# Performance work log

Measured on AMD Instinct MI355X. Metric: run time of the kernel, lower is better.

The kernel has to match this reference:

```python
import jax, jax.numpy as jnp
import numpy as np

B, T, C, HS = 4, 2048, 1024, 64  # batch, seq, n_embd, head_size


def setup_inputs() -> dict:
    key = jax.random.key(0)
    k1, k2, k3, k4 = jax.random.split(key, 4)
    x = jax.random.normal(k1, (B, T, C), dtype=jnp.float32)
    Wq = jax.random.normal(k2, (HS, C), dtype=jnp.float32) * (C ** -0.5)
    Wk = jax.random.normal(k3, (HS, C), dtype=jnp.float32) * (C ** -0.5)
    Wv = jax.random.normal(k4, (HS, C), dtype=jnp.float32) * (C ** -0.5)
    return {"x": x, "Wq": Wq, "Wk": Wk, "Wv": Wv}


def reference(x, Wq, Wk, Wv):
    # q,k,v: [B,T,HS] (nn.Linear: x @ W.T, no bias)
    q = jnp.einsum('btc,hc->bth', x, Wq)
    k = jnp.einsum('btc,hc->bth', x, Wk)
    v = jnp.einsum('btc,hc->bth', x, Wv)
    scale = k.shape[-1] ** -0.5
    wei = jnp.einsum('bth,bsh->bts', q, k) * scale  # [B,T,T]
    # causal mask (tril == 0 -> -inf)
    mask = jnp.tril(jnp.ones((T, T), dtype=bool))
    wei = jnp.where(mask, wei, -jnp.inf)
    wei = jax.nn.softmax(wei, axis=-1)
    # dropout p=0.0 -> identity
    out = jnp.einsum('bts,bsh->bth', wei, v)  # [B,T,HS]
    return out
```

## Files before the change

kernel.cpp:

```cpp
#include <hip/hip_runtime.h>
#include <hip/hip_bf16.h>

#define BB 4
#define TT 2048
#define CC 1024
#define HSZ 64
#define NTOT 8192

typedef __attribute__((ext_vector_type(8))) short bf16x8;
typedef __attribute__((ext_vector_type(4))) float f32x4;

__device__ __forceinline__ unsigned short f2bf(float x) {
    __hip_bfloat16 h = __float2bfloat16(x);
    return *reinterpret_cast<unsigned short*>(&h);
}
__device__ __forceinline__ float bf2f(unsigned short u) {
    return __uint_as_float(((unsigned int)u) << 16);
}

__global__ __launch_bounds__(256) void convert_w(
    const float* __restrict__ Wq, const float* __restrict__ Wk,
    const float* __restrict__ Wv, unsigned short* __restrict__ Wh) {
    int i = blockIdx.x * 256 + threadIdx.x;
    if (i >= 192 * 1024) return;
    int c = i >> 10, kk = i & 1023;
    float val;
    if (c < 64) val = Wq[(size_t)c * CC + kk] * 0.125f;
    else if (c < 128) val = Wk[(size_t)(c - 64) * CC + kk];
    else val = Wv[(size_t)(c - 128) * CC + kk];
    Wh[i] = f2bf(val);
}

__global__ __launch_bounds__(256, 2) void qkv_mfma(
    const float* __restrict__ x, const unsigned short* __restrict__ Wh,
    unsigned short* __restrict__ qs, unsigned short* __restrict__ ksb,
    unsigned short* __restrict__ vT) {
    __shared__ __align__(16) float Pt[4 * 16 * 196];

    const int tid = threadIdx.x;
    const int w = tid >> 6, lane = tid & 63;
    const int l16 = lane & 15, quad = lane >> 4;
    const int row0 = blockIdx.x * 16;
    const int Arow = row0 + l16;

    f32x4 acc[12];
#pragma unroll
    for (int t = 0; t < 12; ++t) acc[t] = (f32x4){0.f, 0.f, 0.f, 0.f};

#pragma unroll
    for (int ch = 0; ch < 4; ++ch) {
        const int kb = w * 256 + ch * 64;
        const float* xp = x + (size_t)Arow * CC + kb;
        float4 xa = *(const float4*)&xp[quad * 8];
        float4 xb = *(const float4*)&xp[quad * 8 + 4];
        float4 xc = *(const float4*)&xp[32 + quad * 8];
        float4 xd = *(const float4*)&xp[32 + quad * 8 + 4];
        bf16x8 ah0, al0, ah1, al1;
        {
            float v0[8] = {xa.x, xa.y, xa.z, xa.w, xb.x, xb.y, xb.z, xb.w};
            float v1[8] = {xc.x, xc.y, xc.z, xc.w, xd.x, xd.y, xd.z, xd.w};
#pragma unroll
            for (int j = 0; j < 8; ++j) {
                unsigned short h = f2bf(v0[j]);
                ah0[j] = (short)h;
                al0[j] = (short)f2bf(v0[j] - bf2f(h));
                unsigned short h2 = f2bf(v1[j]);
                ah1[j] = (short)h2;
                al1[j] = (short)f2bf(v1[j] - bf2f(h2));
            }
        }
#pragma unroll
        for (int nt = 0; nt < 12; ++nt) {
            const unsigned short* Wp = &Wh[(size_t)(nt * 16 + l16) * CC + kb + quad * 8];
            bf16x8 b0 = *(const bf16x8*)Wp;
            bf16x8 b1 = *(const bf16x8*)(Wp + 32);
            f32x4 a = acc[nt];
            a = __builtin_amdgcn_mfma_f32_16x16x32_bf16(ah0, b0, a, 0, 0, 0);
            a = __builtin_amdgcn_mfma_f32_16x16x32_bf16(al0, b0, a, 0, 0, 0);
            a = __builtin_amdgcn_mfma_f32_16x16x32_bf16(ah1, b1, a, 0, 0, 0);
            a = __builtin_amdgcn_mfma_f32_16x16x32_bf16(al1, b1, a, 0, 0, 0);
            acc[nt] = a;
        }
    }
#pragma unroll
    for (int nt = 0; nt < 12; ++nt)
#pragma unroll
        for (int r = 0; r < 4; ++r)
            Pt[(w * 16 + quad * 4 + r) * 196 + nt * 16 + l16] = acc[nt][r];
    __syncthreads();
    for (int e = tid; e < 16 * 192; e += 256) {
        const int row = e / 192, col = e - row * 192;
        float s = 0.f;
#pragma unroll
        for (int kk = 0; kk < 4; ++kk) s += Pt[(kk * 16 + row) * 196 + col];
        unsigned short h = f2bf(s);
        const int grow = row0 + row;
        if (col < 64) qs[(size_t)grow * HSZ + col] = h;
        else if (col < 128) ksb[(size_t)grow * HSZ + (col - 64)] = h;
        else vT[(size_t)(col - 128) * NTOT + grow] = h;
    }
}

__global__ __launch_bounds__(256, 2) void attn_mfma(
    const unsigned short* __restrict__ qs, const unsigned short* __restrict__ ksb,
    const unsigned short* __restrict__ vT, float* __restrict__ out) {
    __shared__ __align__(16) unsigned char smem[17664];
    unsigned short* Ps = (unsigned short*)smem;
    float* Om = (float*)smem;
    float* Lm = (float*)(smem + 17408);

    const int raw = blockIdx.x;
    const int i = (raw < 256) ? raw : 767 - raw;
    const int b = i >> 7;
    const int qt = i & 127;
    const int t0 = qt * 16;
    const int tid = threadIdx.x;
    const int w = tid >> 6, lane = tid & 63;
    const int l16 = lane & 15, quad = lane >> 4;

    const size_t qoff = (size_t)(b * TT + t0 + l16) * HSZ + quad * 8;
    const bf16x8 aq0 = *(const bf16x8*)&qs[qoff];
    const bf16x8 aq1 = *(const bf16x8*)&qs[qoff + 32];

    f32x4 OC[4];
#pragma unroll
    for (int t = 0; t < 4; ++t) OC[t] = (f32x4){0.f, 0.f, 0.f, 0.f};
    float lsum[4] = {0.f, 0.f, 0.f, 0.f};

    const unsigned short* kbase = ksb + (size_t)b * TT * HSZ;
    const int nk = (qt >> 2) + 1;

    bf16x8 ck0[4], ck1[4];
    if (w < nk) {
        const int key0 = w * 64;
#pragma unroll
        for (int nt = 0; nt < 4; ++nt) {
            const unsigned short* kp = kbase + (size_t)(key0 + nt * 16 + l16) * HSZ + quad * 8;
            ck0[nt] = *(const bf16x8*)kp;
            ck1[nt] = *(const bf16x8*)(kp + 32);
        }
    }

    for (int j = w; j < nk; j += 4) {
        const int key0 = j * 64;
        bf16x8 cv0[4], cv1[4];
#pragma unroll
        for (int ht = 0; ht < 4; ++ht) {
            const unsigned short* vp = vT + (size_t)(ht * 16 + l16) * NTOT + b * TT + key0 + quad * 8;
            cv0[ht] = *(const bf16x8*)vp;
            cv1[ht] = *(const bf16x8*)(vp + 32);
        }
        bf16x8 nk0[4], nk1[4];
        const bool more = (j + 4) < nk;
        if (more) {
            const int key0n = key0 + 256;
#pragma unroll
            for (int nt = 0; nt < 4; ++nt) {
                const unsigned short* kp = kbase + (size_t)(key0n + nt * 16 + l16) * HSZ + quad * 8;
                nk0[nt] = *(const bf16x8*)kp;
                nk1[nt] = *(const bf16x8*)(kp + 32);
            }
        }
        f32x4 S[4];
#pragma unroll
        for (int nt = 0; nt < 4; ++nt) {
            f32x4 a = (f32x4){0.f, 0.f, 0.f, 0.f};
            a = __builtin_amdgcn_mfma_f32_16x16x32_bf16(aq0, ck0[nt], a, 0, 0, 0);
            a = __builtin_amdgcn_mfma_f32_16x16x32_bf16(aq1, ck1[nt], a, 0, 0, 0);
            S[nt] = a;
        }
        if (j == nk - 1) {
#pragma unroll
            for (int nt = 0; nt < 4; ++nt) {
                const int key = key0 + nt * 16 + l16;
#pragma unroll
                for (int r = 0; r < 4; ++r)
                    if (key > t0 + quad * 4 + r) S[nt][r] = -1e30f;
            }
        }
#pragma unroll
        for (int nt = 0; nt < 4; ++nt)
#pragma unroll
            for (int r = 0; r < 4; ++r) S[nt][r] = __expf(S[nt][r]);
#pragma unroll
        for (int r = 0; r < 4; ++r)
            lsum[r] += S[0][r] + S[1][r] + S[2][r] + S[3][r];
        unsigned short* Pw = Ps + w * 1152;
#pragma unroll
        for (int nt = 0; nt < 4; ++nt)
#pragma unroll
            for (int r = 0; r < 4; ++r)
                Pw[(quad * 4 + r) * 72 + nt * 16 + l16] = f2bf(S[nt][r]);
        bf16x8 pf0 = *(const bf16x8*)&Pw[l16 * 72 + quad * 8];
        bf16x8 pf1 = *(const bf16x8*)&Pw[l16 * 72 + 32 + quad * 8];
#pragma unroll
        for (int ht = 0; ht < 4; ++ht) {
            f32x4 a = OC[ht];
            a = __builtin_amdgcn_mfma_f32_16x16x32_bf16(pf0, cv0[ht], a, 0, 0, 0);
            a = __builtin_amdgcn_mfma_f32_16x16x32_bf16(pf1, cv1[ht], a, 0, 0, 0);
            OC[ht] = a;
        }
        if (more) {
#pragma unroll
            for (int nt = 0; nt < 4; ++nt) { ck0[nt] = nk0[nt]; ck1[nt] = nk1[nt]; }
        }
    }
#pragma unroll
    for (int r = 0; r < 4; ++r) {
        float v = lsum[r];
#pragma unroll
        for (int off = 1; off < 16; off <<= 1) v += __shfl_xor(v, off, 64);
        lsum[r] = v;
    }
    __syncthreads();
#pragma unroll
    for (int ht = 0; ht < 4; ++ht)
#pragma unroll
        for (int r = 0; r < 4; ++r)
            Om[(w * 16 + quad * 4 + r) * 68 + ht * 16 + l16] = OC[ht][r];
    if (l16 == 0) {
#pragma unroll
        for (int r = 0; r < 4; ++r) Lm[w * 16 + quad * 4 + r] = lsum[r];
    }
    __syncthreads();
    {
        const int row = tid >> 4, h0 = (tid & 15) * 4;
        float L = 0.f, o0 = 0.f, o1 = 0.f, o2 = 0.f, o3 = 0.f;
#pragma unroll
        for (int w2 = 0; w2 < 4; ++w2) {
            L += Lm[w2 * 16 + row];
            const float* p = &Om[(w2 * 16 + row) * 68 + h0];
            o0 += p[0]; o1 += p[1]; o2 += p[2]; o3 += p[3];
        }
        const float inv = 1.f / L;
        *(float4*)&out[(size_t)(b * TT + t0 + row) * HSZ + h0] =
            (float4){o0 * inv, o1 * inv, o2 * inv, o3 * inv};
    }
}

extern "C" void kernel_launch(void* const* d_in, const int* in_sizes, int n_in,
                              void* d_out, int out_size, void* d_ws, size_t ws_size,
                              hipStream_t stream) {
    const float* x  = (const float*)d_in[0];
    const float* Wq = (const float*)d_in[1];
    const float* Wk = (const float*)d_in[2];
    const float* Wv = (const float*)d_in[3];
    float* out = (float*)d_out;

    unsigned short* qs = (unsigned short*)d_ws;
    unsigned short* ksb = qs + (size_t)NTOT * HSZ;
    unsigned short* vT = ksb + (size_t)NTOT * HSZ;
    unsigned short* Wh = vT + (size_t)NTOT * HSZ;

    convert_w<<<768, 256, 0, stream>>>(Wq, Wk, Wv, Wh);
    qkv_mfma<<<512, 256, 0, stream>>>(x, Wh, qs, ksb, vT);
    attn_mfma<<<512, 256, 0, stream>>>(qs, ksb, vT, out);
}
```

Measured before the change: 120.4 us.

## Fuse weight conversion, QKV projection and attention into one cooperative kernel

Merges the three kernels into a single cooperative launch, with grid-wide syncs between weight conversion, QKV projection and attention, to remove two kernel launch gaps. The attention stage also drops the register double-buffered prefetch of K tiles and loads K inline, which lowers register pressure. The costs are grid.sync overhead, a larger shared allocation (50 KB) sized for the projection stage, and a cooperative launch that requires all 512 blocks to be resident at once.

```diff
diff --git a/kernel.cpp b/kernel.cpp
--- a/kernel.cpp
+++ b/kernel.cpp
@@ -1,5 +1,8 @@
 #include <hip/hip_runtime.h>
 #include <hip/hip_bf16.h>
+#include <hip/hip_cooperative_groups.h>
+
+namespace cg = cooperative_groups;
 
 #define BB 4
 #define TT 2048
@@ -18,223 +21,203 @@
     return __uint_as_float(((unsigned int)u) << 16);
 }
 
-__global__ __launch_bounds__(256) void convert_w(
-    const float* __restrict__ Wq, const float* __restrict__ Wk,
-    const float* __restrict__ Wv, unsigned short* __restrict__ Wh) {
-    int i = blockIdx.x * 256 + threadIdx.x;
-    if (i >= 192 * 1024) return;
-    int c = i >> 10, kk = i & 1023;
-    float val;
-    if (c < 64) val = Wq[(size_t)c * CC + kk] * 0.125f;
-    else if (c < 128) val = Wk[(size_t)(c - 64) * CC + kk];
-    else val = Wv[(size_t)(c - 128) * CC + kk];
-    Wh[i] = f2bf(val);
-}
-
-__global__ __launch_bounds__(256, 2) void qkv_mfma(
-    const float* __restrict__ x, const unsigned short* __restrict__ Wh,
+__global__ __launch_bounds__(256, 2) void fused_head(
+    const float* __restrict__ x, const float* __restrict__ Wq,
+    const float* __restrict__ Wk, const float* __restrict__ Wv,
     unsigned short* __restrict__ qs, unsigned short* __restrict__ ksb,
-    unsigned short* __restrict__ vT) {
-    __shared__ __align__(16) float Pt[4 * 16 * 196];
+    unsigned short* __restrict__ vT, unsigned short* __restrict__ Wh,
+    float* __restrict__ out) {
+    __shared__ __align__(16) unsigned char smem[50176];
+    cg::grid_group grid = cg::this_grid();
 
     const int tid = threadIdx.x;
     const int w = tid >> 6, lane = tid & 63;
     const int l16 = lane & 15, quad = lane >> 4;
-    const int row0 = blockIdx.x * 16;
-    const int Arow = row0 + l16;
-
-    f32x4 acc[12];
-#pragma unroll
-    for (int t = 0; t < 12; ++t) acc[t] = (f32x4){0.f, 0.f, 0.f, 0.f};
-
-#pragma unroll
-    for (int ch = 0; ch < 4; ++ch) {
-        const int kb = w * 256 + ch * 64;
-        const float* xp = x + (size_t)Arow * CC + kb;
-        float4 xa = *(const float4*)&xp[quad * 8];
-        float4 xb = *(const float4*)&xp[quad * 8 + 4];
-        float4 xc = *(const float4*)&xp[32 + quad * 8];
-        float4 xd = *(const float4*)&xp[32 + quad * 8 + 4];
-        bf16x8 ah0, al0, ah1, al1;
+
+    for (int i = blockIdx.x * 256 + tid; i < 192 * 1024; i += 512 * 256) {
+        const int c = i >> 10, kk = i & 1023;
+        float val;
+        if (c < 64) val = Wq[(size_t)c * CC + kk] * 0.125f;
+        else if (c < 128) val = Wk[(size_t)(c - 64) * CC + kk];
+        else val = Wv[(size_t)(c - 128) * CC + kk];
+        Wh[i] = f2bf(val);
+    }
+    __threadfence();
+    grid.sync();
+
+    {
+        float* Pt = (float*)smem;
+        const int row0 = blockIdx.x * 16;
+        const int Arow = row0 + l16;
+
+        f32x4 acc[12];
+#pragma unroll
+        for (int t = 0; t < 12; ++t) acc[t] = (f32x4){0.f, 0.f, 0.f, 0.f};
+
+#pragma unroll
+        for (int ch = 0; ch < 4; ++ch) {
+            const int kb = w * 256 + ch * 64;
+            const float* xp = x + (size_t)Arow * CC + kb;
+            float4 xa = *(const float4*)&xp[quad * 8];
+            float4 xb = *(const float4*)&xp[quad * 8 + 4];
+            float4 xc = *(const float4*)&xp[32 + quad * 8];
+            float4 xd = *(const float4*)&xp[32 + quad * 8 + 4];
+            bf16x8 ah0, al0, ah1, al1;
+            {
+                float v0[8] = {xa.x, xa.y, xa.z, xa.w, xb.x, xb.y, xb.z, xb.w};
+                float v1[8] = {xc.x, xc.y, xc.z, xc.w, xd.x, xd.y, xd.z, xd.w};
+#pragma unroll
+                for (int j = 0; j < 8; ++j) {
+                    unsigned short h = f2bf(v0[j]);
+                    ah0[j] = (short)h;
+                    al0[j] = (short)f2bf(v0[j] - bf2f(h));
+                    unsigned short h2 = f2bf(v1[j]);
+                    ah1[j] = (short)h2;
+                    al1[j] = (short)f2bf(v1[j] - bf2f(h2));
+                }
+            }
+#pragma unroll
+            for (int nt = 0; nt < 12; ++nt) {
+                const unsigned short* Wp = &Wh[(size_t)(nt * 16 + l16) * CC + kb + quad * 8];
+                bf16x8 b0 = *(const bf16x8*)Wp;
+                bf16x8 b1 = *(const bf16x8*)(Wp + 32);
+                f32x4 a = acc[nt];
+                a = __builtin_amdgcn_mfma_f32_16x16x32_bf16(ah0, b0, a, 0, 0, 0);
+                a = __builtin_amdgcn_mfma_f32_16x16x32_bf16(al0, b0, a, 0, 0, 0);
+                a = __builtin_amdgcn_mfma_f32_16x16x32_bf16(ah1, b1, a, 0, 0, 0);
+                a = __builtin_amdgcn_mfma_f32_16x16x32_bf16(al1, b1, a, 0, 0, 0);
+                acc[nt] = a;
+            }
+        }
+#pragma unroll
+        for (int nt = 0; nt < 12; ++nt)
+#pragma unroll
+            for (int r = 0; r < 4; ++r)
+                Pt[(w * 16 + quad * 4 + r) * 196 + nt * 16 + l16] = acc[nt][r];
+        __syncthreads();
+        for (int e = tid; e < 16 * 192; e += 256) {
+            const int row = e / 192, col = e - row * 192;
+            float s = 0.f;
+#pragma unroll
+            for (int kk = 0; kk < 4; ++kk) s += Pt[(kk * 16 + row) * 196 + col];
+            unsigned short h = f2bf(s);
+            const int grow = row0 + row;
+            if (col < 64) qs[(size_t)grow * HSZ + col] = h;
+            else if (col < 128) ksb[(size_t)grow * HSZ + (col - 64)] = h;
+            else vT[(size_t)(col - 128) * NTOT + grow] = h;
+        }
+    }
+    __threadfence();
+    grid.sync();
+
+    {
+        unsigned short* Ps = (unsigned short*)smem;
+        float* Om = (float*)smem;
+        float* Lm = (float*)(smem + 17408);
+
+        const int raw = blockIdx.x;
+        const int i = (raw < 256) ? raw : 767 - raw;
+        const int b = i >> 7;
+        const int qt = i & 127;
+        const int t0 = qt * 16;
+
+        const size_t qoff = (size_t)(b * TT + t0 + l16) * HSZ + quad * 8;
+        const bf16x8 aq0 = *(const bf16x8*)&qs[qoff];
+        const bf16x8 aq1 = *(const bf16x8*)&qs[qoff + 32];
+
+        f32x4 OC[4];
+#pragma unroll
+        for (int t = 0; t < 4; ++t) OC[t] = (f32x4){0.f, 0.f, 0.f, 0.f};
+        float lsum[4] = {0.f, 0.f, 0.f, 0.f};
+
+        const unsigned short* kbase = ksb + (size_t)b * TT * HSZ;
+        const int nk = (qt >> 2) + 1;
+
+        for (int j = w; j < nk; j += 4) {
+            const int key0 = j * 64;
+            bf16x8 cv0[4], cv1[4];
+#pragma unroll
+            for (int ht = 0; ht < 4; ++ht) {
+                const unsigned short* vp =
+                    vT + (size_t)(ht * 16 + l16) * NTOT + b * TT + key0 + quad * 8;
+                cv0[ht] = *(const bf16x8*)vp;
+                cv1[ht] = *(const bf16x8*)(vp + 32);
+            }
+            f32x4 S[4];
+#pragma unroll
+            for (int nt = 0; nt < 4; ++nt) {
+                const unsigned short* kp =
+                    kbase + (size_t)(key0 + nt * 16 + l16) * HSZ + quad * 8;
+                bf16x8 bk0 = *(const bf16x8*)kp;
+                bf16x8 bk1 = *(const bf16x8*)(kp + 32);
+                f32x4 a = (f32x4){0.f, 0.f, 0.f, 0.f};
+                a = __builtin_amdgcn_mfma_f32_16x16x32_bf16(aq0, bk0, a, 0, 0, 0);
+                a = __builtin_amdgcn_mfma_f32_16x16x32_bf16(aq1, bk1, a, 0, 0, 0);
+                S[nt] = a;
+            }
+            if (j == nk - 1) {
+#pragma unroll
+                for (int nt = 0; nt < 4; ++nt) {
+                    const int key = key0 + nt * 16 + l16;
+#pragma unroll
+                    for (int r = 0; r < 4; ++r)
+                        if (key > t0 + quad * 4 + r) S[nt][r] = -1e30f;
+                }
+            }
+#pragma unroll
+            for (int nt = 0; nt < 4; ++nt)
+#pragma unroll
+                for (int r = 0; r < 4; ++r) S[nt][r] = __expf(S[nt][r]);
+#pragma unroll
+            for (int r = 0; r < 4; ++r)
+                lsum[r] += S[0][r] + S[1][r] + S[2][r] + S[3][r];
+            unsigned short* Pw = Ps + w * 1152;
+#pragma unroll
+            for (int nt = 0; nt < 4; ++nt)
+#pragma unroll
+                for (int r = 0; r < 4; ++r)
+                    Pw[(quad * 4 + r) * 72 + nt * 16 + l16] = f2bf(S[nt][r]);
+            bf16x8 pf0 = *(const bf16x8*)&Pw[l16 * 72 + quad * 8];
+            bf16x8 pf1 = *(const bf16x8*)&Pw[l16 * 72 + 32 + quad * 8];
+#pragma unroll
+            for (int ht = 0; ht < 4; ++ht) {
+                f32x4 a = OC[ht];
+                a = __builtin_amdgcn_mfma_f32_16x16x32_bf16(pf0, cv0[ht], a, 0, 0, 0);
+                a = __builtin_amdgcn_mfma_f32_16x16x32_bf16(pf1, cv1[ht], a, 0, 0, 0);
+                OC[ht] = a;
+            }
+        }
+#pragma unroll
+        for (int r = 0; r < 4; ++r) {
+            float v = lsum[r];
+#pragma unroll
+            for (int off = 1; off < 16; off <<= 1) v += __shfl_xor(v, off, 64);
+            lsum[r] = v;
+        }
+        __syncthreads();
+#pragma unroll
+        for (int ht = 0; ht < 4; ++ht)
+#pragma unroll
+            for (int r = 0; r < 4; ++r)
+                Om[(w * 16 + quad * 4 + r) * 68 + ht * 16 + l16] = OC[ht][r];
+        if (l16 == 0) {
+#pragma unroll
+            for (int r = 0; r < 4; ++r) Lm[w * 16 + quad * 4 + r] = lsum[r];
+        }
+        __syncthreads();
         {
-            float v0[8] = {xa.x, xa.y, xa.z, xa.w, xb.x, xb.y, xb.z, xb.w};
-            float v1[8] = {xc.x, xc.y, xc.z, xc.w, xd.x, xd.y, xd.z, xd.w};
-#pragma unroll
-            for (int j = 0; j < 8; ++j) {
-                unsigned short h = f2bf(v0[j]);
-                ah0[j] = (short)h;
-                al0[j] = (short)f2bf(v0[j] - bf2f(h));
-                unsigned short h2 = f2bf(v1[j]);
-                ah1[j] = (short)h2;
-                al1[j] = (short)f2bf(v1[j] - bf2f(h2));
-            }
-        }
-#pragma unroll
-        for (int nt = 0; nt < 12; ++nt) {
-            const unsigned short* Wp = &Wh[(size_t)(nt * 16 + l16) * CC + kb + quad * 8];
-            bf16x8 b0 = *(const bf16x8*)Wp;
-            bf16x8 b1 = *(const bf16x8*)(Wp + 32);
-            f32x4 a = acc[nt];
-            a = __builtin_amdgcn_mfma_f32_16x16x32_bf16(ah0, b0, a, 0, 0, 0);
-            a = __builtin_amdgcn_mfma_f32_16x16x32_bf16(al0, b0, a, 0, 0, 0);
-            a = __builtin_amdgcn_mfma_f32_16x16x32_bf16(ah1, b1, a, 0, 0, 0);
-            a = __builtin_amdgcn_mfma_f32_16x16x32_bf16(al1, b1, a, 0, 0, 0);
-            acc[nt] = a;
-        }
-    }
-#pragma unroll
-    for (int nt = 0; nt < 12; ++nt)
-#pragma unroll
-        for (int r = 0; r < 4; ++r)
-            Pt[(w * 16 + quad * 4 + r) * 196 + nt * 16 + l16] = acc[nt][r];
-    __syncthreads();
-    for (int e = tid; e < 16 * 192; e += 256) {
-        const int row = e / 192, col = e - row * 192;
-        float s = 0.f;
-#pragma unroll
-        for (int kk = 0; kk < 4; ++kk) s += Pt[(kk * 16 + row) * 196 + col];
-        unsigned short h = f2bf(s);
-        const int grow = row0 + row;
-        if (col < 64) qs[(size_t)grow * HSZ + col] = h;
-        else if (col < 128) ksb[(size_t)grow * HSZ + (col - 64)] = h;
-        else vT[(size_t)(col - 128) * NTOT + grow] = h;
-    }
-}
-
-__global__ __launch_bounds__(256, 2) void attn_mfma(
-    const unsigned short* __restrict__ qs, const unsigned short* __restrict__ ksb,
-    const unsigned short* __restrict__ vT, float* __restrict__ out) {
-    __shared__ __align__(16) unsigned char smem[17664];
-    unsigned short* Ps = (unsigned short*)smem;
-    float* Om = (float*)smem;
-    float* Lm = (float*)(smem + 17408);
-
-    const int raw = blockIdx.x;
-    const int i = (raw < 256) ? raw : 767 - raw;
-    const int b = i >> 7;
-    const int qt = i & 127;
-    const int t0 = qt * 16;
-    const int tid = threadIdx.x;
-    const int w = tid >> 6, lane = tid & 63;
-    const int l16 = lane & 15, quad = lane >> 4;
-
-    const size_t qoff = (size_t)(b * TT + t0 + l16) * HSZ + quad * 8;
-    const bf16x8 aq0 = *(const bf16x8*)&qs[qoff];
-    const bf16x8 aq1 = *(const bf16x8*)&qs[qoff + 32];
-
-    f32x4 OC[4];
-#pragma unroll
-    for (int t = 0; t < 4; ++t) OC[t] = (f32x4){0.f, 0.f, 0.f, 0.f};
-    float lsum[4] = {0.f, 0.f, 0.f, 0.f};
-
-    const unsigned short* kbase = ksb + (size_t)b * TT * HSZ;
-    const int nk = (qt >> 2) + 1;
-
-    bf16x8 ck0[4], ck1[4];
-    if (w < nk) {
-        const int key0 = w * 64;
-#pragma unroll
-        for (int nt = 0; nt < 4; ++nt) {
-            const unsigned short* kp = kbase + (size_t)(key0 + nt * 16 + l16) * HSZ + quad * 8;
-            ck0[nt] = *(const bf16x8*)kp;
-            ck1[nt] = *(const bf16x8*)(kp + 32);
-        }
-    }
-
-    for (int j = w; j < nk; j += 4) {
-        const int key0 = j * 64;
-        bf16x8 cv0[4], cv1[4];
-#pragma unroll
-        for (int ht = 0; ht < 4; ++ht) {
-            const unsigned short* vp = vT + (size_t)(ht * 16 + l16) * NTOT + b * TT + key0 + quad * 8;
-            cv0[ht] = *(const bf16x8*)vp;
-            cv1[ht] = *(const bf16x8*)(vp + 32);
-        }
-        bf16x8 nk0[4], nk1[4];
-        const bool more = (j + 4) < nk;
-        if (more) {
-            const int key0n = key0 + 256;
-#pragma unroll
-            for (int nt = 0; nt < 4; ++nt) {
-                const unsigned short* kp = kbase + (size_t)(key0n + nt * 16 + l16) * HSZ + quad * 8;
-                nk0[nt] = *(const bf16x8*)kp;
-                nk1[nt] = *(const bf16x8*)(kp + 32);
-            }
-        }
-        f32x4 S[4];
-#pragma unroll
-        for (int nt = 0; nt < 4; ++nt) {
-            f32x4 a = (f32x4){0.f, 0.f, 0.f, 0.f};
-            a = __builtin_amdgcn_mfma_f32_16x16x32_bf16(aq0, ck0[nt], a, 0, 0, 0);
-            a = __builtin_amdgcn_mfma_f32_16x16x32_bf16(aq1, ck1[nt], a, 0, 0, 0);
-            S[nt] = a;
-        }
-        if (j == nk - 1) {
-#pragma unroll
-            for (int nt = 0; nt < 4; ++nt) {
-                const int key = key0 + nt * 16 + l16;
-#pragma unroll
-                for (int r = 0; r < 4; ++r)
-                    if (key > t0 + quad * 4 + r) S[nt][r] = -1e30f;
-            }
-        }
-#pragma unroll
-        for (int nt = 0; nt < 4; ++nt)
-#pragma unroll
-            for (int r = 0; r < 4; ++r) S[nt][r] = __expf(S[nt][r]);
-#pragma unroll
-        for (int r = 0; r < 4; ++r)
-            lsum[r] += S[0][r] + S[1][r] + S[2][r] + S[3][r];
-        unsigned short* Pw = Ps + w * 1152;
-#pragma unroll
-        for (int nt = 0; nt < 4; ++nt)
-#pragma unroll
-            for (int r = 0; r < 4; ++r)
-                Pw[(quad * 4 + r) * 72 + nt * 16 + l16] = f2bf(S[nt][r]);
-        bf16x8 pf0 = *(const bf16x8*)&Pw[l16 * 72 + quad * 8];
-        bf16x8 pf1 = *(const bf16x8*)&Pw[l16 * 72 + 32 + quad * 8];
-#pragma unroll
-        for (int ht = 0; ht < 4; ++ht) {
-            f32x4 a = OC[ht];
-            a = __builtin_amdgcn_mfma_f32_16x16x32_bf16(pf0, cv0[ht], a, 0, 0, 0);
-            a = __builtin_amdgcn_mfma_f32_16x16x32_bf16(pf1, cv1[ht], a, 0, 0, 0);
-            OC[ht] = a;
-        }
-        if (more) {
-#pragma unroll
-            for (int nt = 0; nt < 4; ++nt) { ck0[nt] = nk0[nt]; ck1[nt] = nk1[nt]; }
-        }
-    }
-#pragma unroll
-    for (int r = 0; r < 4; ++r) {
-        float v = lsum[r];
-#pragma unroll
-        for (int off = 1; off < 16; off <<= 1) v += __shfl_xor(v, off, 64);
-        lsum[r] = v;
-    }
-    __syncthreads();
-#pragma unroll
-    for (int ht = 0; ht < 4; ++ht)
-#pragma unroll
-        for (int r = 0; r < 4; ++r)
-            Om[(w * 16 + quad * 4 + r) * 68 + ht * 16 + l16] = OC[ht][r];
-    if (l16 == 0) {
-#pragma unroll
-        for (int r = 0; r < 4; ++r) Lm[w * 16 + quad * 4 + r] = lsum[r];
-    }
-    __syncthreads();
-    {
-        const int row = tid >> 4, h0 = (tid & 15) * 4;
-        float L = 0.f, o0 = 0.f, o1 = 0.f, o2 = 0.f, o3 = 0.f;
-#pragma unroll
-        for (int w2 = 0; w2 < 4; ++w2) {
-            L += Lm[w2 * 16 + row];
-            const float* p = &Om[(w2 * 16 + row) * 68 + h0];
-            o0 += p[0]; o1 += p[1]; o2 += p[2]; o3 += p[3];
-        }
-        const float inv = 1.f / L;
-        *(float4*)&out[(size_t)(b * TT + t0 + row) * HSZ + h0] =
-            (float4){o0 * inv, o1 * inv, o2 * inv, o3 * inv};
+            const int row = tid >> 4, h0 = (tid & 15) * 4;
+            float L = 0.f, o0 = 0.f, o1 = 0.f, o2 = 0.f, o3 = 0.f;
+#pragma unroll
+            for (int w2 = 0; w2 < 4; ++w2) {
+                L += Lm[w2 * 16 + row];
+                const float* p = &Om[(w2 * 16 + row) * 68 + h0];
+                o0 += p[0]; o1 += p[1]; o2 += p[2]; o3 += p[3];
+            }
+            const float inv = 1.f / L;
+            *(float4*)&out[(size_t)(b * TT + t0 + row) * HSZ + h0] =
+                (float4){o0 * inv, o1 * inv, o2 * inv, o3 * inv};
+        }
     }
 }
 
@@ -252,7 +235,8 @@
     unsigned short* vT = ksb + (size_t)NTOT * HSZ;
     unsigned short* Wh = vT + (size_t)NTOT * HSZ;
 
-    convert_w<<<768, 256, 0, stream>>>(Wq, Wk, Wv, Wh);
-    qkv_mfma<<<512, 256, 0, stream>>>(x, Wh, qs, ksb, vT);
-    attn_mfma<<<512, 256, 0, stream>>>(qs, ksb, vT, out);
-}
+    void* args[] = {(void*)&x, (void*)&Wq, (void*)&Wk, (void*)&Wv,
+                    (void*)&qs, (void*)&ksb, (void*)&vT, (void*)&Wh, (void*)&out};
+    hipLaunchCooperativeKernel((const void*)fused_head, dim3(512), dim3(256),
+                               args, 0, stream);
+}
```

After: 352.0 us. 2.92x slower.
